# Performance work log

Measured on AMD Instinct MI355X. Metric: run time of the kernel, lower is better.

The kernel has to match this reference:

```python
import jax, jax.numpy as jnp
import numpy as np

B, N, E, H, ID = 32, 256, 512, 8, 8
D = E // H  # head dim = 64


def setup_inputs() -> dict:
    key = jax.random.key(0)
    ks = jax.random.split(key, 6)
    s = lambda k, shape, fan_in: jax.random.normal(k, shape, jnp.float32) * (fan_in ** -0.5)
    return {
        "x": jax.random.normal(ks[0], (B, N, E), jnp.float32),
        "U": jax.random.normal(ks[1], (B, N, N, ID), jnp.float32),
        "w_qkv": s(ks[2], (3 * E, E), E),   # nn.MultiheadAttention in_proj_weight
        "b_qkv": jnp.zeros((3 * E,), jnp.float32),
        "w_out": s(ks[3], (E, E), E),       # out_proj.weight
        "b_out": jnp.zeros((E,), jnp.float32),
        "w_u": s(ks[4], (H, ID), ID),       # u_proj.weight
        "b_u": jnp.zeros((H,), jnp.float32),
    }


def reference(x, U, w_qkv, b_qkv, w_out, b_out, w_u, b_u):
    # fused QKV projection (torch MHA uses a single in_proj)
    qkv = x @ w_qkv.T + b_qkv                      # [B,N,3E]
    q, k, v = jnp.split(qkv, 3, axis=-1)
    split_heads = lambda t: t.reshape(B, N, H, D).transpose(0, 2, 1, 3)  # [B,H,N,D]
    q, k, v = split_heads(q), split_heads(k), split_heads(v)
    # interaction tensor -> one additive bias per head: [B,N,N,H] -> [B,H,N,N]
    bias = (U @ w_u.T + b_u).transpose(0, 3, 1, 2)
    logits = jnp.einsum('bhnd,bhmd->bhnm', q, k) * (D ** -0.5) + bias  # [B,H,N,N]
    attn = jax.nn.softmax(logits, axis=-1)
    o = jnp.einsum('bhnm,bhmd->bhnd', attn, v)     # [B,H,N,D]
    o = o.transpose(0, 2, 1, 3).reshape(B, N, E)
    return o @ w_out.T + b_out
```

## Files before the change

kernel.cpp:

```cpp
#include <hip/hip_runtime.h>
#include <stdint.h>

#define Bn 32
#define Nn 256
#define En 512
#define Hn 8
#define Dn 64

typedef __attribute__((ext_vector_type(8))) short bf16x8;
typedef __attribute__((ext_vector_type(4))) short bf16x4;
typedef __attribute__((ext_vector_type(4))) float f32x4;
typedef __attribute__((ext_vector_type(4))) _Float16 h4f;

__device__ __forceinline__ unsigned short f2bf(float f){
  union{float f; uint32_t i;} v; v.f = f;
  uint32_t i = v.i;
  return (unsigned short)((i + 0x7fffu + ((i>>16)&1u)) >> 16);
}

__global__ __launch_bounds__(256) void convert_x(
    const float* __restrict__ x, unsigned short* __restrict__ xb){
  size_t i = ((size_t)blockIdx.x * 256 + threadIdx.x) * 8;
  float4 a = *(const float4*)(x + i);
  float4 b = *(const float4*)(x + i + 4);
  bf16x8 p;
  p[0]=(short)f2bf(a.x); p[1]=(short)f2bf(a.y); p[2]=(short)f2bf(a.z); p[3]=(short)f2bf(a.w);
  p[4]=(short)f2bf(b.x); p[5]=(short)f2bf(b.y); p[6]=(short)f2bf(b.z); p[7]=(short)f2bf(b.w);
  *(bf16x8*)(xb + i) = p;
}

__global__ __launch_bounds__(256) void prep_kernel(
    const float* __restrict__ x, unsigned short* __restrict__ xb,
    const float* __restrict__ U, const float* __restrict__ w_u,
    const float* __restrict__ b_u, unsigned short* __restrict__ bias16){
  __shared__ float s_wu[64];
  __shared__ float s_bu[8];
  const int bx = blockIdx.x;
  const int tid = threadIdx.x;
  if (bx < 2048) {
    size_t i = ((size_t)bx * 256 + tid) * 8;
    float4 a = *(const float4*)(x + i);
    float4 b = *(const float4*)(x + i + 4);
    bf16x8 p;
    p[0]=(short)f2bf(a.x); p[1]=(short)f2bf(a.y); p[2]=(short)f2bf(a.z); p[3]=(short)f2bf(a.w);
    p[4]=(short)f2bf(b.x); p[5]=(short)f2bf(b.y); p[6]=(short)f2bf(b.z); p[7]=(short)f2bf(b.w);
    *(bf16x8*)(xb + i) = p;
    return;
  }
  if (tid < 64) s_wu[tid] = w_u[tid];
  if (tid < 8)  s_bu[tid] = b_u[tid];
  __syncthreads();
  const int t  = (bx - 2048) * 256 + tid;
  const int m_ = t & 255;
  const int n4 = (t >> 8) & 63;
  const int bb = t >> 14;
  const float* up = U + ((size_t)(bb*Nn + n4*4)*Nn + m_) * 8;
  float u[4][8];
  #pragma unroll
  for (int r = 0; r < 4; ++r) {
    float4 a = *(const float4*)(up + (size_t)r * (Nn*8));
    float4 c = *(const float4*)(up + (size_t)r * (Nn*8) + 4);
    u[r][0]=a.x; u[r][1]=a.y; u[r][2]=a.z; u[r][3]=a.w;
    u[r][4]=c.x; u[r][5]=c.y; u[r][6]=c.z; u[r][7]=c.w;
  }
  const int    lane_in = ((n4 & 3) * 16 + (m_ & 15)) * 4;
  const size_t tbase   = ((size_t)(n4 >> 2) * 16 + (m_ >> 4)) * 256;
  #pragma unroll
  for (int h = 0; h < 8; ++h) {
    const float bu = s_bu[h];
    float acc[4];
    #pragma unroll
    for (int r = 0; r < 4; ++r) {
      float a = bu;
      #pragma unroll
      for (int id = 0; id < 8; ++id) a += u[r][id] * s_wu[h*8 + id];
      acc[r] = a;
    }
    h4f hv;
    hv[0]=(_Float16)acc[0]; hv[1]=(_Float16)acc[1];
    hv[2]=(_Float16)acc[2]; hv[3]=(_Float16)acc[3];
    *(h4f*)(bias16 + (size_t)(bb*Hn + h) * 65536 + tbase + lane_in) = hv;
  }
}

__global__ __launch_bounds__(256) void qkv_gemm(
    const unsigned short* __restrict__ xb, const float* __restrict__ wq,
    const float* __restrict__ bq,
    unsigned short* __restrict__ q_ws, unsigned short* __restrict__ k_ws,
    unsigned short* __restrict__ v_ws){
  __shared__ unsigned short s_a[128][40];
  __shared__ unsigned short s_b[128][40];
  const int tid = threadIdx.x;
  const int bx = blockIdx.x;
  const int by = blockIdx.y;
  const int row0 = by * 128, n0 = bx * 128;
  const int lane = tid & 63, wv = tid >> 6;
  const int wr = wv >> 1, wc = wv & 1;
  const int lm = lane & 15, quad = lane >> 4;
  const int sr = tid >> 3, sc4 = (tid & 7) * 4;
  f32x4 acc[4][4] = {};
  for (int kc = 0; kc < 16; ++kc) {
    const int k0 = kc * 32;
    __syncthreads();
    #pragma unroll
    for (int i = 0; i < 2; ++i) {
      int g = tid * 2 + i;
      int r = g >> 2, c8 = (g & 3) * 8;
      *(bf16x8*)&s_a[r][c8] = *(const bf16x8*)(xb + (size_t)(row0 + r)*512 + k0 + c8);
    }
    #pragma unroll
    for (int i = 0; i < 4; ++i) {
      int r = sr + i * 32;
      float4 vb = *(const float4*)(wq + (size_t)(n0 + r) * 512 + k0 + sc4);
      bf16x4 pb;
      pb[0]=(short)f2bf(vb.x); pb[1]=(short)f2bf(vb.y); pb[2]=(short)f2bf(vb.z); pb[3]=(short)f2bf(vb.w);
      *(bf16x4*)&s_b[r][sc4] = pb;
    }
    __syncthreads();
    bf16x8 af[4], bfr[4];
    #pragma unroll
    for (int mt = 0; mt < 4; ++mt) af[mt]  = *(const bf16x8*)&s_a[wr*64 + mt*16 + lm][quad*8];
    #pragma unroll
    for (int nt = 0; nt < 4; ++nt) bfr[nt] = *(const bf16x8*)&s_b[wc*64 + nt*16 + lm][quad*8];
    #pragma unroll
    for (int mt = 0; mt < 4; ++mt)
      #pragma unroll
      for (int nt = 0; nt < 4; ++nt)
        acc[mt][nt] = __builtin_amdgcn_mfma_f32_16x16x32_bf16(af[mt], bfr[nt], acc[mt][nt], 0, 0, 0);
  }
  #pragma unroll
  for (int nt = 0; nt < 4; ++nt) {
    int c = n0 + wc*64 + nt*16 + lm;
    float bias = bq[c];
    int sec = c >> 9, ch = c & 511, h = ch >> 6, d = ch & 63;
    #pragma unroll
    for (int mt = 0; mt < 4; ++mt) {
      #pragma unroll
      for (int r = 0; r < 4; ++r) {
        int grow = row0 + wr*64 + mt*16 + quad*4 + r;
        int b = grow >> 8, n = grow & 255;
        float val = acc[mt][nt][r] + bias;
        if (sec == 0)      q_ws[(((size_t)b*Hn + h)*Nn + n)*Dn + d] = f2bf(val * 0.125f);
        else if (sec == 1) k_ws[(((size_t)b*Hn + h)*Nn + n)*Dn + d] = f2bf(val);
        else               v_ws[(((size_t)b*Hn + h)*Dn + d)*Nn + n] = f2bf(val);
      }
    }
  }
}

__global__ __launch_bounds__(256) void attn_fast(
    const unsigned short* __restrict__ bias16,
    const unsigned short* __restrict__ q_ws, const unsigned short* __restrict__ k_ws,
    const unsigned short* __restrict__ v_ws, unsigned short* __restrict__ o_ws){
  __shared__ unsigned short s_p[4][16][40];
  const int tid = threadIdx.x;
  const int wv = tid >> 6, lane = tid & 63;
  const int lm = lane & 15, quad = lane >> 4;
  const int bx = blockIdx.x;
  const int g  = (bx & 7) * 8 + ((bx >> 3) >> 4);
  const int qt = (bx >> 3) & 15;
  const int b = g >> 1, hp = g & 1;
  const int h = hp * 4 + wv;
  const size_t hb = (size_t)b * Hn + h;
  const int qt0 = qt * 16;
  const unsigned short* qp = q_ws + (hb*Nn + qt0 + lm) * Dn;
  const bf16x8 qa0 = *(const bf16x8*)(qp + quad*8);
  const bf16x8 qa1 = *(const bf16x8*)(qp + 32 + quad*8);
  const unsigned short* bt = bias16 + (hb*16 + qt) * 16 * 256 + (size_t)lane*4;
  f32x4 oa[4] = {};
  float m0[4], l0[4];
  #pragma unroll
  for (int r = 0; r < 4; ++r) { m0[r] = -3.0e38f; l0[r] = 0.f; }
  #pragma unroll 1
  for (int ck = 0; ck < 8; ++ck) {
    f32x4 la0, la1;
    #pragma unroll
    for (int t = 0; t < 2; ++t) {
      const int key0 = ck*32 + t*16;
      const h4f hv = *(const h4f*)(bt + (ck*2 + t) * 256);
      f32x4 c0;
      #pragma unroll
      for (int r = 0; r < 4; ++r) c0[r] = (float)hv[r];
      const unsigned short* kp = k_ws + (hb*Nn + key0 + lm) * Dn;
      c0 = __builtin_amdgcn_mfma_f32_16x16x32_bf16(qa0, *(const bf16x8*)(kp + quad*8),      c0, 0, 0, 0);
      c0 = __builtin_amdgcn_mfma_f32_16x16x32_bf16(qa1, *(const bf16x8*)(kp + 32 + quad*8), c0, 0, 0, 0);
      if (t == 0) la0 = c0; else la1 = c0;
    }
    #pragma unroll
    for (int r = 0; r < 4; ++r) {
      float tm = fmaxf(la0[r], la1[r]);
      #pragma unroll
      for (int msk = 1; msk < 16; msk <<= 1) tm = fmaxf(tm, __shfl_xor(tm, msk));
      float mn = fmaxf(m0[r], tm);
      float al = __expf(m0[r] - mn);
      m0[r] = mn;
      float e0 = __expf(la0[r] - mn), e1 = __expf(la1[r] - mn);
      la0[r] = e0; la1[r] = e1;
      float s = e0 + e1;
      #pragma unroll
      for (int msk = 1; msk < 16; msk <<= 1) s += __shfl_xor(s, msk);
      l0[r] = l0[r] * al + s;
      #pragma unroll
      for (int nt = 0; nt < 4; ++nt) oa[nt][r] *= al;
    }
    #pragma unroll
    for (int r = 0; r < 4; ++r) {
      s_p[wv][quad*4+r][lm]      = f2bf(la0[r]);
      s_p[wv][quad*4+r][16 + lm] = f2bf(la1[r]);
    }
    const bf16x8 ap = *(const bf16x8*)&s_p[wv][lm][quad*8];
    #pragma unroll
    for (int nt = 0; nt < 4; ++nt) {
      const bf16x8 bv = *(const bf16x8*)(v_ws + (hb*Dn + nt*16 + lm)*Nn + ck*32 + quad*8);
      oa[nt] = __builtin_amdgcn_mfma_f32_16x16x32_bf16(ap, bv, oa[nt], 0, 0, 0);
    }
  }
  #pragma unroll
  for (int r = 0; r < 4; ++r) {
    const float inv = 1.0f / l0[r];
    const int n = qt0 + quad*4 + r;
    #pragma unroll
    for (int nt = 0; nt < 4; ++nt)
      o_ws[((size_t)(b*Nn + n))*En + h*64 + nt*16 + lm] = f2bf(oa[nt][r] * inv);
  }
}

__global__ __launch_bounds__(256) void attn_kernel(
    const float* __restrict__ U, const float* __restrict__ w_u, const float* __restrict__ b_u,
    const unsigned short* __restrict__ q_ws, const unsigned short* __restrict__ k_ws,
    const unsigned short* __restrict__ v_ws, unsigned short* __restrict__ o_ws){
  __shared__ unsigned short s_p[4][2][16][40];
  __shared__ float s_wu[64];
  __shared__ float s_bu[8];
  const int tid = threadIdx.x;
  const int wv = tid >> 6, lane = tid & 63;
  const int lm = lane & 15, quad = lane >> 4;
  const int blk = blockIdx.x;
  const int b = blk >> 4, qt0 = (blk & 15) * 16;
  if (tid < 64) s_wu[tid] = w_u[tid];
  if (tid < 8)  s_bu[tid] = b_u[tid];
  __syncthreads();
  const int h0 = wv * 2, h1 = h0 + 1;
  const size_t hb0 = (size_t)b * Hn + h0, hb1 = hb0 + 1;
  float wu0[8], wu1[8];
  #pragma unroll
  for (int i = 0; i < 8; ++i) { wu0[i] = s_wu[h0*8 + i]; wu1[i] = s_wu[h1*8 + i]; }
  const float bu0 = s_bu[h0], bu1 = s_bu[h1];
  const unsigned short* q0p = q_ws + (hb0*Nn + qt0 + lm)*Dn;
  const unsigned short* q1p = q_ws + (hb1*Nn + qt0 + lm)*Dn;
  const bf16x8 qa0 = *(const bf16x8*)(q0p + quad*8);
  const bf16x8 qa1 = *(const bf16x8*)(q0p + 32 + quad*8);
  const bf16x8 qb0 = *(const bf16x8*)(q1p + quad*8);
  const bf16x8 qb1 = *(const bf16x8*)(q1p + 32 + quad*8);
  f32x4 oa[4] = {}, ob[4] = {};
  float m0[4], m1[4], l0[4], l1[4];
  #pragma unroll
  for (int r = 0; r < 4; ++r) { m0[r] = m1[r] = -3.0e38f; l0[r] = l1[r] = 0.f; }
  const float* Ub = U + ((size_t)(b*Nn + qt0)) * Nn * 8;
  #pragma unroll 1
  for (int ck = 0; ck < 8; ++ck) {
    f32x4 la0, la1, lb0, lb1;
    #pragma unroll
    for (int t = 0; t < 2; ++t) {
      const int key0 = ck*32 + t*16;
      f32x4 c0, c1;
      #pragma unroll
      for (int r = 0; r < 4; ++r) {
        const float4* up = (const float4*)(Ub + ((size_t)(quad*4+r)*Nn + key0 + lm)*8);
        float4 ua = up[0], uc = up[1];
        c0[r] = bu0 + ua.x*wu0[0] + ua.y*wu0[1] + ua.z*wu0[2] + ua.w*wu0[3]
                    + uc.x*wu0[4] + uc.y*wu0[5] + uc.z*wu0[6] + uc.w*wu0[7];
        c1[r] = bu1 + ua.x*wu1[0] + ua.y*wu1[1] + ua.z*wu1[2] + ua.w*wu1[3]
                    + uc.x*wu1[4] + uc.y*wu1[5] + uc.z*wu1[6] + uc.w*wu1[7];
      }
      const unsigned short* k0p = k_ws + (hb0*Nn + key0 + lm)*Dn;
      const unsigned short* k1p = k_ws + (hb1*Nn + key0 + lm)*Dn;
      bf16x8 kf;
      kf = *(const bf16x8*)(k0p + quad*8);
      c0 = __builtin_amdgcn_mfma_f32_16x16x32_bf16(qa0, kf, c0, 0, 0, 0);
      kf = *(const bf16x8*)(k0p + 32 + quad*8);
      c0 = __builtin_amdgcn_mfma_f32_16x16x32_bf16(qa1, kf, c0, 0, 0, 0);
      kf = *(const bf16x8*)(k1p + quad*8);
      c1 = __builtin_amdgcn_mfma_f32_16x16x32_bf16(qb0, kf, c1, 0, 0, 0);
      kf = *(const bf16x8*)(k1p + 32 + quad*8);
      c1 = __builtin_amdgcn_mfma_f32_16x16x32_bf16(qb1, kf, c1, 0, 0, 0);
      if (t == 0) { la0 = c0; lb0 = c1; } else { la1 = c0; lb1 = c1; }
    }
    #pragma unroll
    for (int r = 0; r < 4; ++r) {
      {
        float tm = fmaxf(la0[r], la1[r]);
        #pragma unroll
        for (int msk = 1; msk < 16; msk <<= 1) tm = fmaxf(tm, __shfl_xor(tm, msk));
        float mn = fmaxf(m0[r], tm);
        float al = __expf(m0[r] - mn);
        m0[r] = mn;
        float e0 = __expf(la0[r] - mn), e1 = __expf(la1[r] - mn);
        la0[r] = e0; la1[r] = e1;
        float s = e0 + e1;
        #pragma unroll
        for (int msk = 1; msk < 16; msk <<= 1) s += __shfl_xor(s, msk);
        l0[r] = l0[r] * al + s;
        #pragma unroll
        for (int nt = 0; nt < 4; ++nt) oa[nt][r] *= al;
      }
      {
        float tm = fmaxf(lb0[r], lb1[r]);
        #pragma unroll
        for (int msk = 1; msk < 16; msk <<= 1) tm = fmaxf(tm, __shfl_xor(tm, msk));
        float mn = fmaxf(m1[r], tm);
        float al = __expf(m1[r] - mn);
        m1[r] = mn;
        float e0 = __expf(lb0[r] - mn), e1 = __expf(lb1[r] - mn);
        lb0[r] = e0; lb1[r] = e1;
        float s = e0 + e1;
        #pragma unroll
        for (int msk = 1; msk < 16; msk <<= 1) s += __shfl_xor(s, msk);
        l1[r] = l1[r] * al + s;
        #pragma unroll
        for (int nt = 0; nt < 4; ++nt) ob[nt][r] *= al;
      }
    }
    #pragma unroll
    for (int r = 0; r < 4; ++r) {
      s_p[wv][0][quad*4+r][lm]      = f2bf(la0[r]);
      s_p[wv][0][quad*4+r][16 + lm] = f2bf(la1[r]);
      s_p[wv][1][quad*4+r][lm]      = f2bf(lb0[r]);
      s_p[wv][1][quad*4+r][16 + lm] = f2bf(lb1[r]);
    }
    const bf16x8 ap0 = *(const bf16x8*)&s_p[wv][0][lm][quad*8];
    const bf16x8 ap1 = *(const bf16x8*)&s_p[wv][1][lm][quad*8];
    #pragma unroll
    for (int nt = 0; nt < 4; ++nt) {
      bf16x8 bv = *(const bf16x8*)(v_ws + (hb0*Dn + nt*16 + lm)*Nn + ck*32 + quad*8);
      oa[nt] = __builtin_amdgcn_mfma_f32_16x16x32_bf16(ap0, bv, oa[nt], 0, 0, 0);
      bv = *(const bf16x8*)(v_ws + (hb1*Dn + nt*16 + lm)*Nn + ck*32 + quad*8);
      ob[nt] = __builtin_amdgcn_mfma_f32_16x16x32_bf16(ap1, bv, ob[nt], 0, 0, 0);
    }
  }
  #pragma unroll
  for (int r = 0; r < 4; ++r) {
    const float i0 = 1.0f / l0[r], i1 = 1.0f / l1[r];
    const int n = qt0 + quad*4 + r;
    #pragma unroll
    for (int nt = 0; nt < 4; ++nt) {
      o_ws[((size_t)(b*Nn + n))*En + h0*64 + nt*16 + lm] = f2bf(oa[nt][r] * i0);
      o_ws[((size_t)(b*Nn + n))*En + h1*64 + nt*16 + lm] = f2bf(ob[nt][r] * i1);
    }
  }
}

__global__ __launch_bounds__(256) void oproj_gemm(
    const unsigned short* __restrict__ o_ws, const float* __restrict__ wo,
    const float* __restrict__ bo, float* __restrict__ out){
  __shared__ unsigned short s_a[128][40];
  __shared__ unsigned short s_b[128][40];
  const int tid = threadIdx.x;
  const int bx = blockIdx.x;
  const int by = blockIdx.y;
  const int row0 = by * 128, n0 = bx * 128;
  const int lane = tid & 63, wv = tid >> 6;
  const int wr = wv >> 1, wc = wv & 1;
  const int lm = lane & 15, quad = lane >> 4;
  const int sr = tid >> 3, sc4 = (tid & 7) * 4;
  f32x4 acc[4][4] = {};
  for (int kc = 0; kc < 16; ++kc) {
    const int k0 = kc * 32;
    __syncthreads();
    #pragma unroll
    for (int i = 0; i < 2; ++i) {
      int g = tid * 2 + i;
      int r = g >> 2, c8 = (g & 3) * 8;
      *(bf16x8*)&s_a[r][c8] = *(const bf16x8*)(o_ws + (size_t)(row0 + r)*512 + k0 + c8);
    }
    #pragma unroll
    for (int i = 0; i < 4; ++i) {
      int r = sr + i * 32;
      float4 vb = *(const float4*)(wo + (size_t)(n0 + r) * 512 + k0 + sc4);
      bf16x4 pb;
      pb[0]=(short)f2bf(vb.x); pb[1]=(short)f2bf(vb.y); pb[2]=(short)f2bf(vb.z); pb[3]=(short)f2bf(vb.w);
      *(bf16x4*)&s_b[r][sc4] = pb;
    }
    __syncthreads();
    bf16x8 af[4], bfr[4];
    #pragma unroll
    for (int mt = 0; mt < 4; ++mt) af[mt]  = *(const bf16x8*)&s_a[wr*64 + mt*16 + lm][quad*8];
    #pragma unroll
    for (int nt = 0; nt < 4; ++nt) bfr[nt] = *(const bf16x8*)&s_b[wc*64 + nt*16 + lm][quad*8];
    #pragma unroll
    for (int mt = 0; mt < 4; ++mt)
      #pragma unroll
      for (int nt = 0; nt < 4; ++nt)
        acc[mt][nt] = __builtin_amdgcn_mfma_f32_16x16x32_bf16(af[mt], bfr[nt], acc[mt][nt], 0, 0, 0);
  }
  #pragma unroll
  for (int nt = 0; nt < 4; ++nt) {
    int c = n0 + wc*64 + nt*16 + lm;
    float bias = bo[c];
    #pragma unroll
    for (int mt = 0; mt < 4; ++mt)
      #pragma unroll
      for (int r = 0; r < 4; ++r) {
        int grow = row0 + wr*64 + mt*16 + quad*4 + r;
        out[(size_t)grow*512 + c] = acc[mt][nt][r] + bias;
      }
  }
}

extern "C" void kernel_launch(void* const* d_in, const int* in_sizes, int n_in,
                              void* d_out, int out_size, void* d_ws, size_t ws_size,
                              hipStream_t stream) {
  const float* x     = (const float*)d_in[0];
  const float* U     = (const float*)d_in[1];
  const float* w_qkv = (const float*)d_in[2];
  const float* b_qkv = (const float*)d_in[3];
  const float* w_out = (const float*)d_in[4];
  const float* b_out = (const float*)d_in[5];
  const float* w_u   = (const float*)d_in[6];
  const float* b_u   = (const float*)d_in[7];
  float* out = (float*)d_out;

  const size_t per = (size_t)Bn * Hn * Nn * Dn;
  unsigned short* q_ws = (unsigned short*)d_ws;
  unsigned short* k_ws = q_ws + per;
  unsigned short* v_ws = k_ws + per;
  unsigned short* o_ws = v_ws + per;
  unsigned short* bias16 = o_ws + per;

  const size_t need = per * 2 * 4 + (size_t)Bn * Hn * Nn * Nn * 2;

  if (ws_size >= need) {
    prep_kernel<<<dim3(4096),  dim3(256), 0, stream>>>(x, o_ws, U, w_u, b_u, bias16);
    qkv_gemm  <<<dim3(12, 64), dim3(256), 0, stream>>>(o_ws, w_qkv, b_qkv, q_ws, k_ws, v_ws);
    attn_fast <<<dim3(1024),   dim3(256), 0, stream>>>(bias16, q_ws, k_ws, v_ws, o_ws);
    oproj_gemm<<<dim3(4, 64),  dim3(256), 0, stream>>>(o_ws, w_out, b_out, out);
  } else {
    convert_x <<<dim3(2048),  dim3(256), 0, stream>>>(x, o_ws);
    qkv_gemm  <<<dim3(12, 64), dim3(256), 0, stream>>>(o_ws, w_qkv, b_qkv, q_ws, k_ws, v_ws);
    attn_kernel<<<dim3(Bn * 16), dim3(256), 0, stream>>>(U, w_u, b_u, q_ws, k_ws, v_ws, o_ws);
    oproj_gemm<<<dim3(4, 64), dim3(256), 0, stream>>>(o_ws, w_out, b_out, out);
  }
}
```

Measured before the change: 219.8 us.

## Pre-convert weights to bf16 and stage GEMM tiles via direct global-to-LDS loads

The prep kernel now also converts w_qkv and w_out to bf16 in extra blocks, so the GEMMs no longer convert fp32 weights in their inner loops. New qkv_gemm2 and oproj_gemm2 kernels use K=64 tiles with an XOR-swizzled LDS layout, filled with global_load_lds 16-byte transfers where that builtin exists. The output projection uses 64-wide N tiles, giving twice as many blocks. The cost is extra weight-conversion work on every call and more workspace, plus reliance on the builtin's wave-base addressing matching the swizzled layout.

```diff
diff --git a/kernel.cpp b/kernel.cpp
--- a/kernel.cpp
+++ b/kernel.cpp
@@ -16,6 +16,20 @@
   union{float f; uint32_t i;} v; v.f = f;
   uint32_t i = v.i;
   return (unsigned short)((i + 0x7fffu + ((i>>16)&1u)) >> 16);
+}
+
+__device__ __forceinline__ void stage16(const unsigned short* g,
+                                        unsigned short* lds_wave_base,
+                                        unsigned short* lds_lane){
+#if __has_builtin(__builtin_amdgcn_global_load_lds)
+  __builtin_amdgcn_global_load_lds(
+      (const __attribute__((address_space(1))) unsigned int*)g,
+      (__attribute__((address_space(3))) unsigned int*)lds_wave_base, 16, 0, 0);
+  (void)lds_lane;
+#else
+  *(bf16x8*)lds_lane = *(const bf16x8*)g;
+  (void)lds_wave_base;
+#endif
 }
 
 __global__ __launch_bounds__(256) void convert_x(
@@ -32,19 +46,24 @@
 __global__ __launch_bounds__(256) void prep_kernel(
     const float* __restrict__ x, unsigned short* __restrict__ xb,
     const float* __restrict__ U, const float* __restrict__ w_u,
-    const float* __restrict__ b_u, unsigned short* __restrict__ bias16){
+    const float* __restrict__ b_u, unsigned short* __restrict__ bias16,
+    const float* __restrict__ wq, unsigned short* __restrict__ wqb,
+    const float* __restrict__ wo, unsigned short* __restrict__ wob){
   __shared__ float s_wu[64];
   __shared__ float s_bu[8];
   const int bx = blockIdx.x;
   const int tid = threadIdx.x;
-  if (bx < 2048) {
-    size_t i = ((size_t)bx * 256 + tid) * 8;
-    float4 a = *(const float4*)(x + i);
-    float4 b = *(const float4*)(x + i + 4);
+  if (bx < 2048 || bx >= 4096) {
+    const float* src; unsigned short* dst; size_t i;
+    if (bx < 2048)      { src = x;  dst = xb;  i = ((size_t)bx * 256 + tid) * 8; }
+    else if (bx < 4480) { src = wq; dst = wqb; i = ((size_t)(bx-4096) * 256 + tid) * 8; }
+    else                { src = wo; dst = wob; i = ((size_t)(bx-4480) * 256 + tid) * 8; }
+    float4 a = *(const float4*)(src + i);
+    float4 b = *(const float4*)(src + i + 4);
     bf16x8 p;
     p[0]=(short)f2bf(a.x); p[1]=(short)f2bf(a.y); p[2]=(short)f2bf(a.z); p[3]=(short)f2bf(a.w);
     p[4]=(short)f2bf(b.x); p[5]=(short)f2bf(b.y); p[6]=(short)f2bf(b.z); p[7]=(short)f2bf(b.w);
-    *(bf16x8*)(xb + i) = p;
+    *(bf16x8*)(dst + i) = p;
     return;
   }
   if (tid < 64) s_wu[tid] = w_u[tid];
@@ -83,13 +102,13 @@
   }
 }
 
-__global__ __launch_bounds__(256) void qkv_gemm(
-    const unsigned short* __restrict__ xb, const float* __restrict__ wq,
+__global__ __launch_bounds__(256) void qkv_gemm2(
+    const unsigned short* __restrict__ xb, const unsigned short* __restrict__ wqb,
     const float* __restrict__ bq,
     unsigned short* __restrict__ q_ws, unsigned short* __restrict__ k_ws,
     unsigned short* __restrict__ v_ws){
-  __shared__ unsigned short s_a[128][40];
-  __shared__ unsigned short s_b[128][40];
+  __shared__ unsigned short s_a[128*64];
+  __shared__ unsigned short s_b[128*64];
   const int tid = threadIdx.x;
   const int bx = blockIdx.x;
   const int by = blockIdx.y;
@@ -97,36 +116,40 @@
   const int lane = tid & 63, wv = tid >> 6;
   const int wr = wv >> 1, wc = wv & 1;
   const int lm = lane & 15, quad = lane >> 4;
-  const int sr = tid >> 3, sc4 = (tid & 7) * 4;
   f32x4 acc[4][4] = {};
-  for (int kc = 0; kc < 16; ++kc) {
-    const int k0 = kc * 32;
-    __syncthreads();
-    #pragma unroll
-    for (int i = 0; i < 2; ++i) {
-      int g = tid * 2 + i;
-      int r = g >> 2, c8 = (g & 3) * 8;
-      *(bf16x8*)&s_a[r][c8] = *(const bf16x8*)(xb + (size_t)(row0 + r)*512 + k0 + c8);
-    }
+  for (int kc = 0; kc < 8; ++kc) {
+    const int k0 = kc * 64;
+    __syncthreads();
     #pragma unroll
     for (int i = 0; i < 4; ++i) {
-      int r = sr + i * 32;
-      float4 vb = *(const float4*)(wq + (size_t)(n0 + r) * 512 + k0 + sc4);
-      bf16x4 pb;
-      pb[0]=(short)f2bf(vb.x); pb[1]=(short)f2bf(vb.y); pb[2]=(short)f2bf(vb.z); pb[3]=(short)f2bf(vb.w);
-      *(bf16x4*)&s_b[r][sc4] = pb;
-    }
-    __syncthreads();
-    bf16x8 af[4], bfr[4];
-    #pragma unroll
-    for (int mt = 0; mt < 4; ++mt) af[mt]  = *(const bf16x8*)&s_a[wr*64 + mt*16 + lm][quad*8];
-    #pragma unroll
-    for (int nt = 0; nt < 4; ++nt) bfr[nt] = *(const bf16x8*)&s_b[wc*64 + nt*16 + lm][quad*8];
-    #pragma unroll
-    for (int mt = 0; mt < 4; ++mt)
-      #pragma unroll
-      for (int nt = 0; nt < 4; ++nt)
-        acc[mt][nt] = __builtin_amdgcn_mfma_f32_16x16x32_bf16(af[mt], bfr[nt], acc[mt][nt], 0, 0, 0);
+      const int ci = i*256 + tid;
+      const int r = ci >> 3, c = ci & 7;
+      const int sc = (c ^ (r & 7)) * 8;
+      unsigned short* wbase_a = s_a + (size_t)(i*256 + wv*64)*8;
+      unsigned short* wbase_b = s_b + (size_t)(i*256 + wv*64)*8;
+      stage16(xb  + (size_t)(row0 + r)*512 + k0 + sc, wbase_a, s_a + (size_t)ci*8);
+      stage16(wqb + (size_t)(n0  + r)*512 + k0 + sc, wbase_b, s_b + (size_t)ci*8);
+    }
+    __syncthreads();
+    #pragma unroll
+    for (int ks = 0; ks < 2; ++ks) {
+      bf16x8 af[4], bfr[4];
+      #pragma unroll
+      for (int mt = 0; mt < 4; ++mt) {
+        const int r = wr*64 + mt*16 + lm;
+        af[mt] = *(const bf16x8*)(s_a + (size_t)r*64 + (((ks*4 + quad) ^ (r & 7)) * 8));
+      }
+      #pragma unroll
+      for (int nt = 0; nt < 4; ++nt) {
+        const int r = wc*64 + nt*16 + lm;
+        bfr[nt] = *(const bf16x8*)(s_b + (size_t)r*64 + (((ks*4 + quad) ^ (r & 7)) * 8));
+      }
+      #pragma unroll
+      for (int mt = 0; mt < 4; ++mt)
+        #pragma unroll
+        for (int nt = 0; nt < 4; ++nt)
+          acc[mt][nt] = __builtin_amdgcn_mfma_f32_16x16x32_bf16(af[mt], bfr[nt], acc[mt][nt], 0, 0, 0);
+    }
   }
   #pragma unroll
   for (int nt = 0; nt < 4; ++nt) {
@@ -145,6 +168,73 @@
         else               v_ws[(((size_t)b*Hn + h)*Dn + d)*Nn + n] = f2bf(val);
       }
     }
+  }
+}
+
+__global__ __launch_bounds__(256) void oproj_gemm2(
+    const unsigned short* __restrict__ o_ws, const unsigned short* __restrict__ wob,
+    const float* __restrict__ bo, float* __restrict__ out){
+  __shared__ unsigned short s_a[128*64];
+  __shared__ unsigned short s_b[64*64];
+  const int tid = threadIdx.x;
+  const int bx = blockIdx.x;
+  const int by = blockIdx.y;
+  const int row0 = by * 128, n0 = bx * 64;
+  const int lane = tid & 63, wv = tid >> 6;
+  const int wr = wv >> 1, wc = wv & 1;
+  const int lm = lane & 15, quad = lane >> 4;
+  f32x4 acc[4][2] = {};
+  for (int kc = 0; kc < 8; ++kc) {
+    const int k0 = kc * 64;
+    __syncthreads();
+    #pragma unroll
+    for (int i = 0; i < 4; ++i) {
+      const int ci = i*256 + tid;
+      const int r = ci >> 3, c = ci & 7;
+      const int sc = (c ^ (r & 7)) * 8;
+      stage16(o_ws + (size_t)(row0 + r)*512 + k0 + sc,
+              s_a + (size_t)(i*256 + wv*64)*8, s_a + (size_t)ci*8);
+    }
+    #pragma unroll
+    for (int i = 0; i < 2; ++i) {
+      const int ci = i*256 + tid;
+      const int r = ci >> 3, c = ci & 7;
+      const int sc = (c ^ (r & 7)) * 8;
+      stage16(wob + (size_t)(n0 + r)*512 + k0 + sc,
+              s_b + (size_t)(i*256 + wv*64)*8, s_b + (size_t)ci*8);
+    }
+    __syncthreads();
+    #pragma unroll
+    for (int ks = 0; ks < 2; ++ks) {
+      bf16x8 af[4], bfr[2];
+      #pragma unroll
+      for (int mt = 0; mt < 4; ++mt) {
+        const int r = wr*64 + mt*16 + lm;
+        af[mt] = *(const bf16x8*)(s_a + (size_t)r*64 + (((ks*4 + quad) ^ (r & 7)) * 8));
+      }
+      #pragma unroll
+      for (int nt = 0; nt < 2; ++nt) {
+        const int r = wc*32 + nt*16 + lm;
+        bfr[nt] = *(const bf16x8*)(s_b + (size_t)r*64 + (((ks*4 + quad) ^ (r & 7)) * 8));
+      }
+      #pragma unroll
+      for (int mt = 0; mt < 4; ++mt)
+        #pragma unroll
+        for (int nt = 0; nt < 2; ++nt)
+          acc[mt][nt] = __builtin_amdgcn_mfma_f32_16x16x32_bf16(af[mt], bfr[nt], acc[mt][nt], 0, 0, 0);
+    }
+  }
+  #pragma unroll
+  for (int nt = 0; nt < 2; ++nt) {
+    int c = n0 + wc*32 + nt*16 + lm;
+    float bias = bo[c];
+    #pragma unroll
+    for (int mt = 0; mt < 4; ++mt)
+      #pragma unroll
+      for (int r = 0; r < 4; ++r) {
+        int grow = row0 + wr*64 + mt*16 + quad*4 + r;
+        out[(size_t)grow*512 + c] = acc[mt][nt][r] + bias;
+      }
   }
 }
 
@@ -225,6 +315,71 @@
   }
 }
 
+__global__ __launch_bounds__(256) void qkv_gemm(
+    const unsigned short* __restrict__ xb, const float* __restrict__ wq,
+    const float* __restrict__ bq,
+    unsigned short* __restrict__ q_ws, unsigned short* __restrict__ k_ws,
+    unsigned short* __restrict__ v_ws){
+  __shared__ unsigned short s_a[128][40];
+  __shared__ unsigned short s_b[128][40];
+  const int tid = threadIdx.x;
+  const int bx = blockIdx.x;
+  const int by = blockIdx.y;
+  const int row0 = by * 128, n0 = bx * 128;
+  const int lane = tid & 63, wv = tid >> 6;
+  const int wr = wv >> 1, wc = wv & 1;
+  const int lm = lane & 15, quad = lane >> 4;
+  const int sr = tid >> 3, sc4 = (tid & 7) * 4;
+  f32x4 acc[4][4] = {};
+  for (int kc = 0; kc < 16; ++kc) {
+    const int k0 = kc * 32;
+    __syncthreads();
+    #pragma unroll
+    for (int i = 0; i < 2; ++i) {
+      int g = tid * 2 + i;
+      int r = g >> 2, c8 = (g & 3) * 8;
+      *(bf16x8*)&s_a[r][c8] = *(const bf16x8*)(xb + (size_t)(row0 + r)*512 + k0 + c8);
+    }
+    #pragma unroll
+    for (int i = 0; i < 4; ++i) {
+      int r = sr + i * 32;
+      float4 vb = *(const float4*)(wq + (size_t)(n0 + r) * 512 + k0 + sc4);
+      bf16x4 pb;
+      pb[0]=(short)f2bf(vb.x); pb[1]=(short)f2bf(vb.y); pb[2]=(short)f2bf(vb.z); pb[3]=(short)f2bf(vb.w);
+      *(bf16x4*)&s_b[r][sc4] = pb;
+    }
+    __syncthreads();
+    bf16x8 af[4], bfr[4];
+    #pragma unroll
+    for (int mt = 0; mt < 4; ++mt) af[mt]  = *(const bf16x8*)&s_a[wr*64 + mt*16 + lm][quad*8];
+    #pragma unroll
+    for (int nt = 0; nt < 4; ++nt) bfr[nt] = *(const bf16x8*)&s_b[wc*64 + nt*16 + lm][quad*8];
+    #pragma unroll
+    for (int mt = 0; mt < 4; ++mt)
+      #pragma unroll
+      for (int nt = 0; nt < 4; ++nt)
+        acc[mt][nt] = __builtin_amdgcn_mfma_f32_16x16x32_bf16(af[mt], bfr[nt], acc[mt][nt], 0, 0, 0);
+  }
+  #pragma unroll
+  for (int nt = 0; nt < 4; ++nt) {
+    int c = n0 + wc*64 + nt*16 + lm;
+    float bias = bq[c];
+    int sec = c >> 9, ch = c & 511, h = ch >> 6, d = ch & 63;
+    #pragma unroll
+    for (int mt = 0; mt < 4; ++mt) {
+      #pragma unroll
+      for (int r = 0; r < 4; ++r) {
+        int grow = row0 + wr*64 + mt*16 + quad*4 + r;
+        int b = grow >> 8, n = grow & 255;
+        float val = acc[mt][nt][r] + bias;
+        if (sec == 0)      q_ws[(((size_t)b*Hn + h)*Nn + n)*Dn + d] = f2bf(val * 0.125f);
+        else if (sec == 1) k_ws[(((size_t)b*Hn + h)*Nn + n)*Dn + d] = f2bf(val);
+        else               v_ws[(((size_t)b*Hn + h)*Dn + d)*Nn + n] = f2bf(val);
+      }
+    }
+  }
+}
+
 __global__ __launch_bounds__(256) void attn_kernel(
     const float* __restrict__ U, const float* __restrict__ w_u, const float* __restrict__ b_u,
     const unsigned short* __restrict__ q_ws, const unsigned short* __restrict__ k_ws,
@@ -426,14 +581,17 @@
   unsigned short* v_ws = k_ws + per;
   unsigned short* o_ws = v_ws + per;
   unsigned short* bias16 = o_ws + per;
-
-  const size_t need = per * 2 * 4 + (size_t)Bn * Hn * Nn * Nn * 2;
+  unsigned short* wqb = bias16 + (size_t)Bn*Hn*Nn*Nn;
+  unsigned short* wob = wqb + (size_t)3*En*En;
+
+  const size_t need = (per*4 + (size_t)Bn*Hn*Nn*Nn + (size_t)3*En*En + (size_t)En*En) * 2;
 
   if (ws_size >= need) {
-    prep_kernel<<<dim3(4096),  dim3(256), 0, stream>>>(x, o_ws, U, w_u, b_u, bias16);
-    qkv_gemm  <<<dim3(12, 64), dim3(256), 0, stream>>>(o_ws, w_qkv, b_qkv, q_ws, k_ws, v_ws);
+    prep_kernel<<<dim3(4608),  dim3(256), 0, stream>>>(x, o_ws, U, w_u, b_u, bias16,
+                                                       w_qkv, wqb, w_out, wob);
+    qkv_gemm2 <<<dim3(12, 64), dim3(256), 0, stream>>>(o_ws, wqb, b_qkv, q_ws, k_ws, v_ws);
     attn_fast <<<dim3(1024),   dim3(256), 0, stream>>>(bias16, q_ws, k_ws, v_ws, o_ws);
-    oproj_gemm<<<dim3(4, 64),  dim3(256), 0, stream>>>(o_ws, w_out, b_out, out);
+    oproj_gemm2<<<dim3(8, 64), dim3(256), 0, stream>>>(o_ws, wob, b_out, out);
   } else {
     convert_x <<<dim3(2048),  dim3(256), 0, stream>>>(x, o_ws);
     qkv_gemm  <<<dim3(12, 64), dim3(256), 0, stream>>>(o_ws, w_qkv, b_qkv, q_ws, k_ws, v_ws);
```

New measurement: 216.8 us. About the same (-1.3%).
